# Performance work log

Measured on AMD Instinct MI355X. Metric: run time of the kernel, lower is better.

## Reference

```python
import jax, jax.numpy as jnp
import numpy as np

V, E, H, B, S = 32000, 512, 1024, 128, 512
NEG = -1e9


def setup_inputs() -> dict:
    key = jax.random.key(0)
    ks = jax.random.split(key, 12)
    s = 0.02
    return {
        "previous_word": jax.random.randint(ks[0], (B, 1), 0, V),
        "h_0": jax.random.normal(ks[1], (B, H), jnp.float32),
        "c_0": jax.random.normal(ks[2], (B, H), jnp.float32),
        "ctx": jax.random.normal(ks[3], (B, S, H), jnp.float32),
        "ctx_mask": jnp.zeros((B, S), dtype=bool),
        "emb": jax.random.normal(ks[4], (V, E), jnp.float32) * s,
        "W_ih": jax.random.normal(ks[5], (4 * H, E), jnp.float32) * s,
        "W_hh": jax.random.normal(ks[6], (4 * H, H), jnp.float32) * s,
        "b_ih": jnp.zeros((4 * H,), jnp.float32),
        "b_hh": jnp.zeros((4 * H,), jnp.float32),
        "W_in": jax.random.normal(ks[7], (H, H), jnp.float32) * s,
        "W_out": jax.random.normal(ks[8], (H, 2 * H), jnp.float32) * s,
        "W_dec": jax.random.normal(ks[9], (V, H), jnp.float32) * s,
        "b_dec": jnp.zeros((V,), jnp.float32),
    }


def reference(previous_word, h_0, c_0, ctx, ctx_mask, emb, W_ih, W_hh, b_ih, b_hh, W_in, W_out, W_dec, b_dec):
    # embedding lookup + squeeze; dropout is identity in eval mode
    x = emb[previous_word[:, 0]]                       # [B, E]
    # LSTMCell: gate order i, f, g, o (PyTorch convention)
    gates = x @ W_ih.T + b_ih + h_0 @ W_hh.T + b_hh    # [B, 4H]
    i, f, g, o = jnp.split(gates, 4, axis=1)
    i = jax.nn.sigmoid(i)
    f = jax.nn.sigmoid(f)
    g = jnp.tanh(g)
    o = jax.nn.sigmoid(o)
    c_1 = f * c_0 + i * g
    h_1 = o * jnp.tanh(c_1)
    # SoftDotAttention
    target = h_1 @ W_in.T                               # [B, H]
    attn = jnp.einsum('bsh,bh->bs', ctx, target)        # [B, S]
    attn = jnp.where(ctx_mask, NEG, attn)
    alpha = jax.nn.softmax(attn, axis=1)
    weighted = jnp.einsum('bs,bsh->bh', alpha, ctx)     # [B, H]
    h_tilde = jnp.tanh(jnp.concatenate([weighted, h_1], axis=1) @ W_out.T)
    logit = h_tilde @ W_dec.T + b_dec                   # [B, V]
    return (h_1, c_1, alpha, logit)
```

## Files before the change

### kernel.cpp

```cpp
#include <hip/hip_runtime.h>
#include <hip/hip_bf16.h>
#include <cstdint>

#define NEG_BIG (-1.0e9f)

typedef __attribute__((ext_vector_type(8))) short short8_t;
typedef __attribute__((ext_vector_type(4))) float f32x4;

typedef __attribute__((address_space(1))) const unsigned int gu32_t;
typedef __attribute__((address_space(3))) unsigned int lu32_t;

__device__ __forceinline__ short f2bf(float x) {
  union { float f; unsigned u; } v; v.f = x;
  unsigned r = v.u + 0x7fffu + ((v.u >> 16) & 1u);
  return (short)(r >> 16);
}
__device__ __forceinline__ float sigmoidf_(float x) { return 1.0f / (1.0f + __expf(-x)); }

__device__ __forceinline__ void lds_barrier() {
  asm volatile("s_waitcnt lgkmcnt(0)\n\ts_barrier" ::: "memory");
}
__device__ __forceinline__ void block_barrier() {
  asm volatile("" ::: "memory");
  __builtin_amdgcn_s_barrier();
  asm volatile("" ::: "memory");
}

__launch_bounds__(256, 2)
__global__ void k_ggemm2(const int* __restrict__ prev, const float* __restrict__ emb,
                         const float* __restrict__ h0,
                         const float* __restrict__ W_ih, const float* __restrict__ W_hh,
                         float* __restrict__ gp) {
  __shared__ __align__(16) short lA[2][128 * 64];
  __shared__ __align__(16) short lW[2][16 * 64];
  const int kc = blockIdx.z, nblk = blockIdx.x;
  const int tid = threadIdx.x;
  const int wid = tid >> 6, l = tid & 63, l15 = l & 15, khalf = l >> 4;
  const int kbase = kc * 384;

  const int arow = tid >> 1, apart = tid & 1;
  const int aswz = (arow & 7) << 4;
  const float* embrow = emb + (size_t)prev[arow] * 512;
  const float* h0row = h0 + (size_t)arow * 1024;

  const int wn = (tid * 4) >> 6, wkq = (tid * 4) & 63;
  const float* wih = W_ih + (size_t)(nblk * 16 + wn) * 512;
  const float* whh = W_hh + (size_t)(nblk * 16 + wn) * 1024;

  f32x4 acc[2];
  acc[0] = (f32x4){0.f, 0.f, 0.f, 0.f};
  acc[1] = (f32x4){0.f, 0.f, 0.f, 0.f};

  float4 aF[8], wR;
  auto stage_regs = [&](int k0) {
    const int col0 = kbase + k0 + apart * 32;
    const float* asrc = (col0 < 512) ? (embrow + col0) : (h0row + (col0 - 512));
#pragma unroll
    for (int q = 0; q < 8; ++q) aF[q] = *(const float4*)(asrc + q * 4);
    const int kg = kbase + k0 + wkq;
    wR = (kg < 512) ? *(const float4*)(wih + kg) : *(const float4*)(whh + (kg - 512));
  };
  auto write_lds = [&](int buf) {
    char* drow = (char*)lA[buf] + arow * 128;
#pragma unroll
    for (int q = 0; q < 4; ++q) {
      short8_t s;
      s[0] = f2bf(aF[2 * q].x); s[1] = f2bf(aF[2 * q].y);
      s[2] = f2bf(aF[2 * q].z); s[3] = f2bf(aF[2 * q].w);
      s[4] = f2bf(aF[2 * q + 1].x); s[5] = f2bf(aF[2 * q + 1].y);
      s[6] = f2bf(aF[2 * q + 1].z); s[7] = f2bf(aF[2 * q + 1].w);
      *(short8_t*)(drow + ((apart * 64 + q * 16) ^ aswz)) = s;
    }
    short4 h4;
    h4.x = f2bf(wR.x); h4.y = f2bf(wR.y); h4.z = f2bf(wR.z); h4.w = f2bf(wR.w);
    *(short4*)((char*)lW[buf] + wn * 128 + ((wkq * 2) ^ ((wn & 7) << 4))) = h4;
  };
  auto compute = [&](int buf) {
#pragma unroll
    for (int ks = 0; ks < 2; ++ks) {
      const int ubyte = ks * 64 + khalf * 16;
      short8_t bfrag = *(const short8_t*)((char*)lW[buf] + l15 * 128 + (ubyte ^ ((l15 & 7) << 4)));
#pragma unroll
      for (int r = 0; r < 2; ++r) {
        const int mrow = wid * 32 + r * 16 + l15;
        short8_t afrag = *(const short8_t*)((char*)lA[buf] + mrow * 128 + (ubyte ^ ((mrow & 7) << 4)));
        acc[r] = __builtin_amdgcn_mfma_f32_16x16x32_bf16(afrag, bfrag, acc[r], 0, 0, 0);
      }
    }
  };

  stage_regs(0);
  write_lds(0);
  for (int t = 0; t < 6; ++t) {
    const int cur = t & 1;
    if (t + 1 < 6) stage_regs((t + 1) << 6);
    lds_barrier();
    compute(cur);
    if (t + 1 < 6) write_lds(cur ^ 1);
  }

  const int n = nblk * 16 + l15;
  float* out = gp + (size_t)kc * 524288;
#pragma unroll
  for (int r = 0; r < 2; ++r) {
    int mb = wid * 32 + r * 16 + khalf * 4;
#pragma unroll
    for (int e = 0; e < 4; ++e)
      out[(size_t)(mb + e) * 4096 + n] = acc[r][e];
  }
}

__global__ void k_lstm2(const float* __restrict__ gp, const float* __restrict__ b_ih,
                        const float* __restrict__ b_hh, const float* __restrict__ c0,
                        float* __restrict__ h1_out, float* __restrict__ c1_out,
                        short* __restrict__ A3) {
  int t = blockIdx.x * 256 + threadIdx.x;
  int b = t >> 10, h = t & 1023;
  float iv = b_ih[h] + b_hh[h];
  float fv = b_ih[1024 + h] + b_hh[1024 + h];
  float gv = b_ih[2048 + h] + b_hh[2048 + h];
  float ov = b_ih[3072 + h] + b_hh[3072 + h];
#pragma unroll
  for (int kc = 0; kc < 4; ++kc) {
    const float* g = gp + (size_t)kc * 524288 + (size_t)b * 4096;
    iv += g[h]; fv += g[1024 + h]; gv += g[2048 + h]; ov += g[3072 + h];
  }
  float c1 = sigmoidf_(fv) * c0[t] + sigmoidf_(iv) * tanhf(gv);
  float h1 = sigmoidf_(ov) * tanhf(c1);
  c1_out[t] = c1;
  h1_out[t] = h1;
  A3[(size_t)b * 2048 + 1024 + h] = f2bf(h1);
}

template <int MB, int WN, int EPI>
__launch_bounds__(256, 2)
__global__ void k_gemm(const short* __restrict__ A, int lda,
                       const float* __restrict__ Wa, int ldwa, int Ka,
                       const float* __restrict__ Wb, int ldwb, int Ktot,
                       const float* __restrict__ bias0, const float* __restrict__ bias1,
                       float* __restrict__ outF, short* __restrict__ outB, int ldo,
                       int kstride, size_t pstride) {
  constexpr int BN = WN * 16;
  constexpr int MREP = (MB == 128) ? 2 * WN : 1;
  constexpr int AU = MB / 32;
  constexpr int WLOADS = (BN * 64) / 1024;
  __shared__ __align__(16) short lA[2][MB * 64];
  __shared__ __align__(16) short lW[2][BN * 64];
  const int kc = blockIdx.z;
  A += (size_t)kc * kstride;
  Wa += (size_t)kc * kstride;
  if (outF) outF += (size_t)kc * pstride;
  const int tid = threadIdx.x;
  const int wid = tid >> 6, l = tid & 63, l15 = l & 15, khalf = l >> 4;
  const int nblk = blockIdx.x;
  const int mrow0 = blockIdx.y * MB;
  const int m_wave = (WN == 1) ? wid * (MB / 4) : 0;
  const int nb_local = (WN == 4) ? wid * 16 : 0;

  const int arow = (MB == 128) ? (tid >> 1) : (tid >> 2);
  const int apart = (MB == 128) ? (tid & 1) : (tid & 3);
  const int abase = apart * (AU * 16);
  const int aswz = (arow & 7) << 4;
  const short* Arow = A + (size_t)(mrow0 + arow) * lda + apart * (AU * 8);

  int wn_[WLOADS], wkq_[WLOADS];
#pragma unroll
  for (int j = 0; j < WLOADS; ++j) {
    int idx = j * 1024 + tid * 4;
    wn_[j] = idx >> 6;
    wkq_[j] = idx & 63;
  }

  f32x4 acc[MREP];
#pragma unroll
  for (int r = 0; r < MREP; ++r) acc[r] = (f32x4){0.f, 0.f, 0.f, 0.f};

  short8_t aR[AU];
  float4 wR[WLOADS];

  auto stage_regs = [&](int k0) {
#pragma unroll
    for (int q = 0; q < AU; ++q) aR[q] = *(const short8_t*)(Arow + k0 + q * 8);
#pragma unroll
    for (int j = 0; j < WLOADS; ++j) {
      int kg = k0 + wkq_[j];
      const float* p = (kg < Ka) ? (Wa + (size_t)(nblk * BN + wn_[j]) * ldwa + kg)
                                 : (Wb + (size_t)(nblk * BN + wn_[j]) * ldwb + (kg - Ka));
      wR[j] = *(const float4*)p;
    }
  };
  auto write_lds = [&](int buf) {
    char* drow = (char*)lA[buf] + arow * 128;
#pragma unroll
    for (int q = 0; q < AU; ++q)
      *(short8_t*)(drow + ((abase + q * 16) ^ aswz)) = aR[q];
#pragma unroll
    for (int j = 0; j < WLOADS; ++j) {
      short4 h4;
      h4.x = f2bf(wR[j].x); h4.y = f2bf(wR[j].y); h4.z = f2bf(wR[j].z); h4.w = f2bf(wR[j].w);
      *(short4*)((char*)lW[buf] + wn_[j] * 128 + ((wkq_[j] * 2) ^ ((wn_[j] & 7) << 4))) = h4;
    }
  };
  auto compute = [&](int buf) {
#pragma unroll
    for (int ks = 0; ks < 2; ++ks) {
      const int ubyte = ks * 64 + khalf * 16;
      const int nrow = nb_local + l15;
      short8_t bfrag = *(const short8_t*)((char*)lW[buf] + nrow * 128 + (ubyte ^ ((nrow & 7) << 4)));
#pragma unroll
      for (int r = 0; r < MREP; ++r) {
        const int mrow = m_wave + r * 16 + l15;
        short8_t afrag = *(const short8_t*)((char*)lA[buf] + mrow * 128 + (ubyte ^ ((mrow & 7) << 4)));
        acc[r] = __builtin_amdgcn_mfma_f32_16x16x32_bf16(afrag, bfrag, acc[r], 0, 0, 0);
      }
    }
  };

  const int NT = Ktot >> 6;
  stage_regs(0);
  write_lds(0);
  for (int t = 0; t < NT; ++t) {
    const int cur = t & 1;
    if (t + 1 < NT) stage_regs((t + 1) << 6);
    lds_barrier();
    compute(cur);
    if (t + 1 < NT) write_lds(cur ^ 1);
  }

  const int n = nblk * BN + nb_local + l15;
  float bias = 0.f;
  if (bias0) bias = bias0[n];
  if (bias1) bias += bias1[n];
#pragma unroll
  for (int r = 0; r < MREP; ++r) {
    int mb = mrow0 + m_wave + r * 16 + khalf * 4;
#pragma unroll
    for (int e = 0; e < 4; ++e) {
      float v = acc[r][e] + bias;
      if (EPI == 1) {
        outB[(size_t)(mb + e) * ldo + n] = f2bf(tanhf(v));
      } else {
        outF[(size_t)(mb + e) * ldo + n] = v;
      }
    }
  }
}

__launch_bounds__(256, 2)
__global__ void k_attn(const float* __restrict__ ctx, const float* __restrict__ tp,
                       const unsigned char* __restrict__ mask,
                       float* __restrict__ scores, float* __restrict__ part) {
  __shared__ __align__(16) float lds[2][8 * 1024];
  __shared__ float sml[8];
  const int b = blockIdx.x >> 2, chunk = blockIdx.x & 3;
  const int tid = threadIdx.x;
  const int wid = tid >> 6, l = tid & 63;
  float4 t4[4], w4[4];
#pragma unroll
  for (int j = 0; j < 4; ++j) {
    float4 a = {0.f, 0.f, 0.f, 0.f};
#pragma unroll
    for (int p = 0; p < 4; ++p) {
      const float4 v = *(const float4*)(tp + (size_t)p * 131072 + (size_t)b * 1024 + j * 256 + l * 4);
      a.x += v.x; a.y += v.y; a.z += v.z; a.w += v.w;
    }
    t4[j] = a;
    w4[j].x = 0.f; w4[j].y = 0.f; w4[j].z = 0.f; w4[j].w = 0.f;
  }
  float m = -INFINITY, lsum = 0.f;
  const int s0 = chunk * 128;
  const float* cb = ctx + ((size_t)b * 512 + s0) * 1024;
  const unsigned char* mk = mask + (size_t)b * 512 + s0;

  auto stage = [&](int buf, int tt) {
    const char* src = (const char*)(cb + (size_t)tt * 8192);
    char* dst = (char*)&lds[buf][0];
#pragma unroll
    for (int i = 0; i < 8; ++i) {
      const int off = i * 4096 + tid * 16;
      __builtin_amdgcn_global_load_lds((gu32_t*)(src + off), (lu32_t*)(dst + off), 16, 0, 0);
    }
  };

  stage(0, 0);
  int buf = 0;
  for (int t = 0; t < 16; ++t) {
    if (t < 15) {
      stage(buf ^ 1, t + 1);
      asm volatile("s_waitcnt vmcnt(8)" ::: "memory");
    } else {
      asm volatile("s_waitcnt vmcnt(0)" ::: "memory");
    }
    block_barrier();
#pragma unroll
    for (int rr = 0; rr < 2; ++rr) {
      const int r = wid * 2 + rr;
      const float* row = &lds[buf][r * 1024];
      float4 c0 = *(const float4*)(row + l * 4);
      float4 c1 = *(const float4*)(row + 256 + l * 4);
      float4 c2 = *(const float4*)(row + 512 + l * 4);
      float4 c3 = *(const float4*)(row + 768 + l * 4);
      float p = c0.x * t4[0].x + c0.y * t4[0].y + c0.z * t4[0].z + c0.w * t4[0].w +
                c1.x * t4[1].x + c1.y * t4[1].y + c1.z * t4[1].z + c1.w * t4[1].w +
                c2.x * t4[2].x + c2.y * t4[2].y + c2.z * t4[2].z + c2.w * t4[2].w +
                c3.x * t4[3].x + c3.y * t4[3].y + c3.z * t4[3].z + c3.w * t4[3].w;
#pragma unroll
      for (int off = 32; off > 0; off >>= 1) p += __shfl_xor(p, off);
      const int sg = t * 8 + r;
      if (mk[sg]) p = NEG_BIG;
      if (l == 0) scores[(size_t)b * 512 + s0 + sg] = p;
      float mn = fmaxf(m, p);
      float scale = __expf(m - mn);
      float e = __expf(p - mn);
      lsum = lsum * scale + e;
      w4[0].x = w4[0].x * scale + e * c0.x; w4[0].y = w4[0].y * scale + e * c0.y;
      w4[0].z = w4[0].z * scale + e * c0.z; w4[0].w = w4[0].w * scale + e * c0.w;
      w4[1].x = w4[1].x * scale + e * c1.x; w4[1].y = w4[1].y * scale + e * c1.y;
      w4[1].z = w4[1].z * scale + e * c1.z; w4[1].w = w4[1].w * scale + e * c1.w;
      w4[2].x = w4[2].x * scale + e * c2.x; w4[2].y = w4[2].y * scale + e * c2.y;
      w4[2].z = w4[2].z * scale + e * c2.z; w4[2].w = w4[2].w * scale + e * c2.w;
      w4[3].x = w4[3].x * scale + e * c3.x; w4[3].y = w4[3].y * scale + e * c3.y;
      w4[3].z = w4[3].z * scale + e * c3.z; w4[3].w = w4[3].w * scale + e * c3.w;
      m = mn;
    }
    block_barrier();
    buf ^= 1;
  }

  float* cbuf = &lds[0][0];
#pragma unroll
  for (int j = 0; j < 4; ++j) *(float4*)(cbuf + wid * 1024 + j * 256 + l * 4) = w4[j];
  if (l == 0) { sml[wid] = m; sml[4 + wid] = lsum; }
  __syncthreads();
  const float M = fmaxf(fmaxf(sml[0], sml[1]), fmaxf(sml[2], sml[3]));
  const float sc0 = __expf(sml[0] - M), sc1 = __expf(sml[1] - M);
  const float sc2 = __expf(sml[2] - M), sc3 = __expf(sml[3] - M);
  const float L = sml[4] * sc0 + sml[5] * sc1 + sml[6] * sc2 + sml[7] * sc3;
  const float4 v0 = *(const float4*)(cbuf + 0 * 1024 + tid * 4);
  const float4 v1 = *(const float4*)(cbuf + 1 * 1024 + tid * 4);
  const float4 v2 = *(const float4*)(cbuf + 2 * 1024 + tid * 4);
  const float4 v3 = *(const float4*)(cbuf + 3 * 1024 + tid * 4);
  float4 o;
  o.x = v0.x * sc0 + v1.x * sc1 + v2.x * sc2 + v3.x * sc3;
  o.y = v0.y * sc0 + v1.y * sc1 + v2.y * sc2 + v3.y * sc3;
  o.z = v0.z * sc0 + v1.z * sc1 + v2.z * sc2 + v3.z * sc3;
  o.w = v0.w * sc0 + v1.w * sc1 + v2.w * sc2 + v3.w * sc3;
  float* pp = part + ((size_t)b * 4 + chunk) * 1028;
  *(float4*)(pp + tid * 4) = o;
  if (tid == 0) { pp[1024] = M; pp[1025] = L; }
}

__launch_bounds__(256, 4)
__global__ void k_finish(const float* __restrict__ scores, const float* __restrict__ part,
                         float* __restrict__ alpha, short* __restrict__ A3) {
  __shared__ float sm[4], sl[4];
  int b = blockIdx.x, t = threadIdx.x;
  if (t < 4) {
    sm[t] = part[((size_t)b * 4 + t) * 1028 + 1024];
    sl[t] = part[((size_t)b * 4 + t) * 1028 + 1025];
  }
  __syncthreads();
  float M = fmaxf(fmaxf(sm[0], sm[1]), fmaxf(sm[2], sm[3]));
  float scl[4];
  float L = 0.f;
#pragma unroll
  for (int i = 0; i < 4; ++i) {
    scl[i] = __expf(sm[i] - M);
    L += sl[i] * scl[i];
  }
  float inv = 1.0f / L;
  float s0 = scores[(size_t)b * 512 + t];
  float s1 = scores[(size_t)b * 512 + 256 + t];
  alpha[(size_t)b * 512 + t] = __expf(s0 - M) * inv;
  alpha[(size_t)b * 512 + 256 + t] = __expf(s1 - M) * inv;
  float ax = 0.f, ay = 0.f, az = 0.f, aw = 0.f;
#pragma unroll
  for (int i = 0; i < 4; ++i) {
    const float4 w = *(const float4*)(part + ((size_t)b * 4 + i) * 1028 + t * 4);
    ax += scl[i] * w.x; ay += scl[i] * w.y; az += scl[i] * w.z; aw += scl[i] * w.w;
  }
  short4 o4;
  o4.x = f2bf(ax * inv); o4.y = f2bf(ay * inv); o4.z = f2bf(az * inv); o4.w = f2bf(aw * inv);
  *(short4*)(A3 + (size_t)b * 2048 + t * 4) = o4;
}

__global__ void k_htilde(const float* __restrict__ wp, short* __restrict__ ht) {
  int t = blockIdx.x * 256 + threadIdx.x;
  float s = 0.f;
#pragma unroll
  for (int p = 0; p < 8; ++p) s += wp[(size_t)p * 131072 + t];
  ht[t] = f2bf(tanhf(s));
}

extern "C" void kernel_launch(void* const* d_in, const int* in_sizes, int n_in,
                              void* d_out, int out_size, void* d_ws, size_t ws_size,
                              hipStream_t stream) {
  const int* prev = (const int*)d_in[0];
  const float* h0 = (const float*)d_in[1];
  const float* c0 = (const float*)d_in[2];
  const float* ctx = (const float*)d_in[3];
  const unsigned char* mask = (const unsigned char*)d_in[4];
  const float* emb = (const float*)d_in[5];
  const float* W_ih = (const float*)d_in[6];
  const float* W_hh = (const float*)d_in[7];
  const float* b_ih = (const float*)d_in[8];
  const float* b_hh = (const float*)d_in[9];
  const float* W_in = (const float*)d_in[10];
  const float* W_out = (const float*)d_in[11];
  const float* W_dec = (const float*)d_in[12];
  const float* b_dec = (const float*)d_in[13];

  float* out_h1 = (float*)d_out;
  float* out_c1 = out_h1 + 128 * 1024;
  float* out_alpha = out_c1 + 128 * 1024;
  float* out_logit = out_alpha + 128 * 512;

  char* ws = (char*)d_ws;
  short* A3 = (short*)(ws + 0x000000);
  float* scores = (float*)(ws + 0x100000);
  float* tp = (float*)(ws + 0x200000);
  float* part = (float*)(ws + 0x400000);
  float* wp = (float*)(ws + 0x700000);
  float* gp = (float*)(ws + 0xB00000);
  short* htilde = (short*)(ws + 0x1300000);

  k_ggemm2<<<dim3(256, 1, 4), 256, 0, stream>>>(prev, emb, h0, W_ih, W_hh, gp);
  k_lstm2<<<512, 256, 0, stream>>>(gp, b_ih, b_hh, c0, out_h1, out_c1, A3);
  k_gemm<128, 1, 0><<<dim3(64, 1, 4), 256, 0, stream>>>(
      A3 + 1024, 2048, W_in, 1024, 1 << 30, W_in, 1024, 256, nullptr, nullptr, tp, nullptr,
      1024, 256, (size_t)131072);
  k_attn<<<512, 256, 0, stream>>>(ctx, tp, mask, scores, part);
  k_finish<<<128, 256, 0, stream>>>(scores, part, out_alpha, A3);
  k_gemm<128, 1, 0><<<dim3(64, 1, 8), 256, 0, stream>>>(
      A3, 2048, W_out, 2048, 1 << 30, W_out, 2048, 256, nullptr, nullptr, wp, nullptr,
      1024, 256, (size_t)131072);
  k_htilde<<<512, 256, 0, stream>>>(wp, htilde);
  k_gemm<128, 4, 0><<<dim3(500, 1, 1), 256, 0, stream>>>(
      htilde, 1024, W_dec, 1024, 1024, W_dec, 1024, 1024, b_dec, nullptr, out_logit, nullptr,
      32000, 0, 0);
}
```

Baseline: 139.7 us.

## Fuse split-K reductions into producer kernels via last-block atomic counters

Removes the separate LSTM-elementwise, attention-finish and htilde-reduction kernels. Each producer kernel increments a per-tile atomic counter after writing its partials, and the last-arriving block does the reduction and epilogue. A tiny zeroing kernel resets the counters each call. This cuts three launches and their round trips, at the cost of threadfences, atomics and a serial tail done by the single last block per tile.

```diff
diff --git a/kernel.cpp b/kernel.cpp
--- a/kernel.cpp
+++ b/kernel.cpp
@@ -26,13 +26,20 @@
   asm volatile("" ::: "memory");
 }
 
+__global__ void k_zero(unsigned int* __restrict__ c) { c[threadIdx.x] = 0u; }
+
 __launch_bounds__(256, 2)
 __global__ void k_ggemm2(const int* __restrict__ prev, const float* __restrict__ emb,
                          const float* __restrict__ h0,
                          const float* __restrict__ W_ih, const float* __restrict__ W_hh,
-                         float* __restrict__ gp) {
+                         const float* __restrict__ b_ih, const float* __restrict__ b_hh,
+                         const float* __restrict__ c0,
+                         float* __restrict__ h1_out, float* __restrict__ c1_out,
+                         short* __restrict__ A3,
+                         float* __restrict__ gp, unsigned int* __restrict__ ctr) {
   __shared__ __align__(16) short lA[2][128 * 64];
   __shared__ __align__(16) short lW[2][16 * 64];
+  __shared__ int isLast;
   const int kc = blockIdx.z, nblk = blockIdx.x;
   const int tid = threadIdx.x;
   const int wid = tid >> 6, l = tid & 63, l15 = l & 15, khalf = l >> 4;
@@ -108,28 +115,36 @@
     for (int e = 0; e < 4; ++e)
       out[(size_t)(mb + e) * 4096 + n] = acc[r][e];
   }
-}
-
-__global__ void k_lstm2(const float* __restrict__ gp, const float* __restrict__ b_ih,
-                        const float* __restrict__ b_hh, const float* __restrict__ c0,
-                        float* __restrict__ h1_out, float* __restrict__ c1_out,
-                        short* __restrict__ A3) {
-  int t = blockIdx.x * 256 + threadIdx.x;
-  int b = t >> 10, h = t & 1023;
-  float iv = b_ih[h] + b_hh[h];
-  float fv = b_ih[1024 + h] + b_hh[1024 + h];
-  float gv = b_ih[2048 + h] + b_hh[2048 + h];
-  float ov = b_ih[3072 + h] + b_hh[3072 + h];
-#pragma unroll
-  for (int kc = 0; kc < 4; ++kc) {
-    const float* g = gp + (size_t)kc * 524288 + (size_t)b * 4096;
-    iv += g[h]; fv += g[1024 + h]; gv += g[2048 + h]; ov += g[3072 + h];
-  }
-  float c1 = sigmoidf_(fv) * c0[t] + sigmoidf_(iv) * tanhf(gv);
-  float h1 = sigmoidf_(ov) * tanhf(c1);
-  c1_out[t] = c1;
-  h1_out[t] = h1;
-  A3[(size_t)b * 2048 + 1024 + h] = f2bf(h1);
+
+  const int hb = nblk & 63;
+  __threadfence();
+  __syncthreads();
+  if (tid == 0) isLast = (atomicAdd(&ctr[hb], 1u) == 15u);
+  __syncthreads();
+  if (isLast) {
+    __threadfence();
+    const int hbase = hb * 16;
+#pragma unroll
+    for (int q = 0; q < 8; ++q) {
+      int idx = q * 256 + tid;
+      int b = idx >> 4, hl = idx & 15;
+      int h = hbase + hl;
+      float g4[4];
+#pragma unroll
+      for (int g = 0; g < 4; ++g) {
+        float s = b_ih[g * 1024 + h] + b_hh[g * 1024 + h];
+#pragma unroll
+        for (int k2 = 0; k2 < 4; ++k2)
+          s += gp[(size_t)k2 * 524288 + (size_t)b * 4096 + g * 1024 + h];
+        g4[g] = s;
+      }
+      float c1 = sigmoidf_(g4[1]) * c0[b * 1024 + h] + sigmoidf_(g4[0]) * tanhf(g4[2]);
+      float h1 = sigmoidf_(g4[3]) * tanhf(c1);
+      c1_out[b * 1024 + h] = c1;
+      h1_out[b * 1024 + h] = h1;
+      A3[(size_t)b * 2048 + 1024 + h] = f2bf(h1);
+    }
+  }
 }
 
 template <int MB, int WN, int EPI>
@@ -249,9 +264,12 @@
 __launch_bounds__(256, 2)
 __global__ void k_attn(const float* __restrict__ ctx, const float* __restrict__ tp,
                        const unsigned char* __restrict__ mask,
-                       float* __restrict__ scores, float* __restrict__ part) {
+                       float* __restrict__ scores, float* __restrict__ part,
+                       float* __restrict__ alpha, short* __restrict__ A3,
+                       unsigned int* __restrict__ ctr) {
   __shared__ __align__(16) float lds[2][8 * 1024];
   __shared__ float sml[8];
+  __shared__ int isLast;
   const int b = blockIdx.x >> 2, chunk = blockIdx.x & 3;
   const int tid = threadIdx.x;
   const int wid = tid >> 6, l = tid & 63;
@@ -332,64 +350,146 @@
   for (int j = 0; j < 4; ++j) *(float4*)(cbuf + wid * 1024 + j * 256 + l * 4) = w4[j];
   if (l == 0) { sml[wid] = m; sml[4 + wid] = lsum; }
   __syncthreads();
-  const float M = fmaxf(fmaxf(sml[0], sml[1]), fmaxf(sml[2], sml[3]));
-  const float sc0 = __expf(sml[0] - M), sc1 = __expf(sml[1] - M);
-  const float sc2 = __expf(sml[2] - M), sc3 = __expf(sml[3] - M);
-  const float L = sml[4] * sc0 + sml[5] * sc1 + sml[6] * sc2 + sml[7] * sc3;
-  const float4 v0 = *(const float4*)(cbuf + 0 * 1024 + tid * 4);
-  const float4 v1 = *(const float4*)(cbuf + 1 * 1024 + tid * 4);
-  const float4 v2 = *(const float4*)(cbuf + 2 * 1024 + tid * 4);
-  const float4 v3 = *(const float4*)(cbuf + 3 * 1024 + tid * 4);
-  float4 o;
-  o.x = v0.x * sc0 + v1.x * sc1 + v2.x * sc2 + v3.x * sc3;
-  o.y = v0.y * sc0 + v1.y * sc1 + v2.y * sc2 + v3.y * sc3;
-  o.z = v0.z * sc0 + v1.z * sc1 + v2.z * sc2 + v3.z * sc3;
-  o.w = v0.w * sc0 + v1.w * sc1 + v2.w * sc2 + v3.w * sc3;
-  float* pp = part + ((size_t)b * 4 + chunk) * 1028;
-  *(float4*)(pp + tid * 4) = o;
-  if (tid == 0) { pp[1024] = M; pp[1025] = L; }
-}
-
-__launch_bounds__(256, 4)
-__global__ void k_finish(const float* __restrict__ scores, const float* __restrict__ part,
-                         float* __restrict__ alpha, short* __restrict__ A3) {
-  __shared__ float sm[4], sl[4];
-  int b = blockIdx.x, t = threadIdx.x;
-  if (t < 4) {
-    sm[t] = part[((size_t)b * 4 + t) * 1028 + 1024];
-    sl[t] = part[((size_t)b * 4 + t) * 1028 + 1025];
-  }
-  __syncthreads();
-  float M = fmaxf(fmaxf(sm[0], sm[1]), fmaxf(sm[2], sm[3]));
-  float scl[4];
-  float L = 0.f;
-#pragma unroll
-  for (int i = 0; i < 4; ++i) {
-    scl[i] = __expf(sm[i] - M);
-    L += sl[i] * scl[i];
-  }
-  float inv = 1.0f / L;
-  float s0 = scores[(size_t)b * 512 + t];
-  float s1 = scores[(size_t)b * 512 + 256 + t];
-  alpha[(size_t)b * 512 + t] = __expf(s0 - M) * inv;
-  alpha[(size_t)b * 512 + 256 + t] = __expf(s1 - M) * inv;
-  float ax = 0.f, ay = 0.f, az = 0.f, aw = 0.f;
-#pragma unroll
-  for (int i = 0; i < 4; ++i) {
-    const float4 w = *(const float4*)(part + ((size_t)b * 4 + i) * 1028 + t * 4);
-    ax += scl[i] * w.x; ay += scl[i] * w.y; az += scl[i] * w.z; aw += scl[i] * w.w;
-  }
-  short4 o4;
-  o4.x = f2bf(ax * inv); o4.y = f2bf(ay * inv); o4.z = f2bf(az * inv); o4.w = f2bf(aw * inv);
-  *(short4*)(A3 + (size_t)b * 2048 + t * 4) = o4;
-}
-
-__global__ void k_htilde(const float* __restrict__ wp, short* __restrict__ ht) {
-  int t = blockIdx.x * 256 + threadIdx.x;
-  float s = 0.f;
-#pragma unroll
-  for (int p = 0; p < 8; ++p) s += wp[(size_t)p * 131072 + t];
-  ht[t] = f2bf(tanhf(s));
+  {
+    const float M = fmaxf(fmaxf(sml[0], sml[1]), fmaxf(sml[2], sml[3]));
+    const float sc0 = __expf(sml[0] - M), sc1 = __expf(sml[1] - M);
+    const float sc2 = __expf(sml[2] - M), sc3 = __expf(sml[3] - M);
+    const float L = sml[4] * sc0 + sml[5] * sc1 + sml[6] * sc2 + sml[7] * sc3;
+    const float4 v0 = *(const float4*)(cbuf + 0 * 1024 + tid * 4);
+    const float4 v1 = *(const float4*)(cbuf + 1 * 1024 + tid * 4);
+    const float4 v2 = *(const float4*)(cbuf + 2 * 1024 + tid * 4);
+    const float4 v3 = *(const float4*)(cbuf + 3 * 1024 + tid * 4);
+    float4 o;
+    o.x = v0.x * sc0 + v1.x * sc1 + v2.x * sc2 + v3.x * sc3;
+    o.y = v0.y * sc0 + v1.y * sc1 + v2.y * sc2 + v3.y * sc3;
+    o.z = v0.z * sc0 + v1.z * sc1 + v2.z * sc2 + v3.z * sc3;
+    o.w = v0.w * sc0 + v1.w * sc1 + v2.w * sc2 + v3.w * sc3;
+    float* pp = part + ((size_t)b * 4 + chunk) * 1028;
+    *(float4*)(pp + tid * 4) = o;
+    if (tid == 0) { pp[1024] = M; pp[1025] = L; }
+  }
+
+  __threadfence();
+  __syncthreads();
+  if (tid == 0) isLast = (atomicAdd(&ctr[b], 1u) == 3u);
+  __syncthreads();
+  if (isLast) {
+    __threadfence();
+    const float* ps = part + (size_t)b * 4 * 1028;
+    const float m0 = ps[1024], l0 = ps[1025];
+    const float m1 = ps[1028 + 1024], l1 = ps[1028 + 1025];
+    const float m2 = ps[2056 + 1024], l2 = ps[2056 + 1025];
+    const float m3 = ps[3084 + 1024], l3 = ps[3084 + 1025];
+    const float M = fmaxf(fmaxf(m0, m1), fmaxf(m2, m3));
+    const float s0e = __expf(m0 - M), s1e = __expf(m1 - M);
+    const float s2e = __expf(m2 - M), s3e = __expf(m3 - M);
+    const float inv = 1.0f / (l0 * s0e + l1 * s1e + l2 * s2e + l3 * s3e);
+    const float sa = scores[(size_t)b * 512 + tid];
+    const float sb = scores[(size_t)b * 512 + 256 + tid];
+    alpha[(size_t)b * 512 + tid] = __expf(sa - M) * inv;
+    alpha[(size_t)b * 512 + 256 + tid] = __expf(sb - M) * inv;
+    const float4 v0 = *(const float4*)(ps + tid * 4);
+    const float4 v1 = *(const float4*)(ps + 1028 + tid * 4);
+    const float4 v2 = *(const float4*)(ps + 2056 + tid * 4);
+    const float4 v3 = *(const float4*)(ps + 3084 + tid * 4);
+    short4 o4;
+    o4.x = f2bf((v0.x * s0e + v1.x * s1e + v2.x * s2e + v3.x * s3e) * inv);
+    o4.y = f2bf((v0.y * s0e + v1.y * s1e + v2.y * s2e + v3.y * s3e) * inv);
+    o4.z = f2bf((v0.z * s0e + v1.z * s1e + v2.z * s2e + v3.z * s3e) * inv);
+    o4.w = f2bf((v0.w * s0e + v1.w * s1e + v2.w * s2e + v3.w * s3e) * inv);
+    *(short4*)(A3 + (size_t)b * 2048 + tid * 4) = o4;
+  }
+}
+
+__launch_bounds__(256, 2)
+__global__ void k_wout(const short* __restrict__ A3, const float* __restrict__ W_out,
+                       float* __restrict__ wp, short* __restrict__ ht,
+                       unsigned int* __restrict__ ctr) {
+  __shared__ __align__(16) short lA[2][128 * 64];
+  __shared__ __align__(16) short lW[2][16 * 64];
+  __shared__ int isLast;
+  const int kc = blockIdx.z, nblk = blockIdx.x;
+  const int tid = threadIdx.x;
+  const int wid = tid >> 6, l = tid & 63, l15 = l & 15, khalf = l >> 4;
+
+  const int arow = tid >> 1, apart = tid & 1;
+  const int aswz = (arow & 7) << 4;
+  const short* Arow = A3 + (size_t)arow * 2048 + kc * 256 + apart * 32;
+
+  const int wn = (tid * 4) >> 6, wkq = (tid * 4) & 63;
+  const float* wrow = W_out + (size_t)(nblk * 16 + wn) * 2048 + kc * 256;
+
+  f32x4 acc[2];
+  acc[0] = (f32x4){0.f, 0.f, 0.f, 0.f};
+  acc[1] = (f32x4){0.f, 0.f, 0.f, 0.f};
+
+  short8_t aR[4];
+  float4 wR;
+  auto stage_regs = [&](int k0) {
+#pragma unroll
+    for (int q = 0; q < 4; ++q) aR[q] = *(const short8_t*)(Arow + k0 + q * 8);
+    wR = *(const float4*)(wrow + k0 + wkq);
+  };
+  auto write_lds = [&](int buf) {
+    char* drow = (char*)lA[buf] + arow * 128;
+#pragma unroll
+    for (int q = 0; q < 4; ++q)
+      *(short8_t*)(drow + ((apart * 64 + q * 16) ^ aswz)) = aR[q];
+    short4 h4;
+    h4.x = f2bf(wR.x); h4.y = f2bf(wR.y); h4.z = f2bf(wR.z); h4.w = f2bf(wR.w);
+    *(short4*)((char*)lW[buf] + wn * 128 + ((wkq * 2) ^ ((wn & 7) << 4))) = h4;
+  };
+  auto compute = [&](int buf) {
+#pragma unroll
+    for (int ks = 0; ks < 2; ++ks) {
+      const int ubyte = ks * 64 + khalf * 16;
+      short8_t bfrag = *(const short8_t*)((char*)lW[buf] + l15 * 128 + (ubyte ^ ((l15 & 7) << 4)));
+#pragma unroll
+      for (int r = 0; r < 2; ++r) {
+        const int mrow = wid * 32 + r * 16 + l15;
+        short8_t afrag = *(const short8_t*)((char*)lA[buf] + mrow * 128 + (ubyte ^ ((mrow & 7) << 4)));
+        acc[r] = __builtin_amdgcn_mfma_f32_16x16x32_bf16(afrag, bfrag, acc[r], 0, 0, 0);
+      }
+    }
+  };
+
+  stage_regs(0);
+  write_lds(0);
+  for (int t = 0; t < 4; ++t) {
+    const int cur = t & 1;
+    if (t + 1 < 4) stage_regs((t + 1) << 6);
+    lds_barrier();
+    compute(cur);
+    if (t + 1 < 4) write_lds(cur ^ 1);
+  }
+
+  const int n = nblk * 16 + l15;
+  float* out = wp + (size_t)kc * 131072;
+#pragma unroll
+  for (int r = 0; r < 2; ++r) {
+    int mb = wid * 32 + r * 16 + khalf * 4;
+#pragma unroll
+    for (int e = 0; e < 4; ++e)
+      out[(size_t)(mb + e) * 1024 + n] = acc[r][e];
+  }
+
+  __threadfence();
+  __syncthreads();
+  if (tid == 0) isLast = (atomicAdd(&ctr[nblk], 1u) == 7u);
+  __syncthreads();
+  if (isLast) {
+    __threadfence();
+#pragma unroll
+    for (int q = 0; q < 8; ++q) {
+      int idx = q * 256 + tid;
+      int m = idx >> 4, nl = idx & 15;
+      float s = 0.f;
+#pragma unroll
+      for (int p = 0; p < 8; ++p)
+        s += wp[(size_t)p * 131072 + (size_t)m * 1024 + nblk * 16 + nl];
+      ht[(size_t)m * 1024 + nblk * 16 + nl] = f2bf(tanhf(s));
+    }
+  }
 }
 
 extern "C" void kernel_launch(void* const* d_in, const int* in_sizes, int n_in,
@@ -423,18 +523,16 @@
   float* wp = (float*)(ws + 0x700000);
   float* gp = (float*)(ws + 0xB00000);
   short* htilde = (short*)(ws + 0x1300000);
-
-  k_ggemm2<<<dim3(256, 1, 4), 256, 0, stream>>>(prev, emb, h0, W_ih, W_hh, gp);
-  k_lstm2<<<512, 256, 0, stream>>>(gp, b_ih, b_hh, c0, out_h1, out_c1, A3);
+  unsigned int* ctrs = (unsigned int*)(ws + 0x1340000);
+
+  k_zero<<<1, 256, 0, stream>>>(ctrs);
+  k_ggemm2<<<dim3(256, 1, 4), 256, 0, stream>>>(prev, emb, h0, W_ih, W_hh, b_ih, b_hh, c0,
+                                                out_h1, out_c1, A3, gp, ctrs);
   k_gemm<128, 1, 0><<<dim3(64, 1, 4), 256, 0, stream>>>(
       A3 + 1024, 2048, W_in, 1024, 1 << 30, W_in, 1024, 256, nullptr, nullptr, tp, nullptr,
       1024, 256, (size_t)131072);
-  k_attn<<<512, 256, 0, stream>>>(ctx, tp, mask, scores, part);
-  k_finish<<<128, 256, 0, stream>>>(scores, part, out_alpha, A3);
-  k_gemm<128, 1, 0><<<dim3(64, 1, 8), 256, 0, stream>>>(
-      A3, 2048, W_out, 2048, 1 << 30, W_out, 2048, 256, nullptr, nullptr, wp, nullptr,
-      1024, 256, (size_t)131072);
-  k_htilde<<<512, 256, 0, stream>>>(wp, htilde);
+  k_attn<<<512, 256, 0, stream>>>(ctx, tp, mask, scores, part, out_alpha, A3, ctrs + 64);
+  k_wout<<<dim3(64, 1, 8), 256, 0, stream>>>(A3, W_out, wp, htilde, ctrs + 192);
   k_gemm<128, 4, 0><<<dim3(500, 1, 1), 256, 0, stream>>>(
       htilde, 1024, W_dec, 1024, 1024, W_dec, 1024, 1024, b_dec, nullptr, out_logit, nullptr,
       32000, 0, 0);
```

After: 395.8 us. 2.83x slower.
